# Kernel tuning notes

Measured on AMD Instinct MI355X. Metric: run time of the kernel, lower is better.

The kernel has to match this reference:

```python
import jax, jax.numpy as jnp
import numpy as np

N_HEADS = 16
HEAD_DIM = 64
ROPE_BASE = 10000.0


def _apply_rope(x, offset):
    # x: (B, T, H, hd); rotates consecutive pairs (x[2i], x[2i+1]) as complex numbers,
    # matching torch.view_as_complex on reshape(..., -1, 2).
    B, T, H, hd = x.shape
    inv_freq = 1.0 / (ROPE_BASE ** (jnp.arange(0, hd, 2, dtype=jnp.float32) / hd))  # (hd/2,)
    t = jnp.arange(T, dtype=jnp.float32) + offset
    ang = t[:, None] * inv_freq[None, :]                      # (T, hd/2)
    cos = jnp.cos(ang)[None, :, None, :]                      # (1, T, 1, hd/2)
    sin = jnp.sin(ang)[None, :, None, :]
    x1 = x[..., 0::2]
    x2 = x[..., 1::2]
    out = jnp.stack([x1 * cos - x2 * sin, x1 * sin + x2 * cos], axis=-1)
    return out.reshape(B, T, H, hd).astype(x.dtype)


def setup_inputs() -> dict:
    key = jax.random.key(0)
    ks = jax.random.split(key, 5)
    D = N_HEADS * HEAD_DIM  # 1024
    s = 1.0 / np.sqrt(D)
    x = jax.random.normal(ks[0], (2, 2048, D), jnp.float32)
    Wqkv = jax.random.normal(ks[1], (D, 3 * D), jnp.float32) * s
    bqkv = jax.random.normal(ks[2], (3 * D,), jnp.float32) * 0.01
    Wout = jax.random.normal(ks[3], (D, D), jnp.float32) * s
    bout = jax.random.normal(ks[4], (D,), jnp.float32) * 0.01
    return {"x": x, "Wqkv": Wqkv, "bqkv": bqkv, "Wout": Wout, "bout": bout, "offset": 0}


def reference(x, Wqkv, bqkv, Wout, bout, offset):
    B, T, D = x.shape
    qkv = (x @ Wqkv + bqkv).reshape(B, T, 3, N_HEADS, HEAD_DIM)
    q, k, v = qkv[:, :, 0], qkv[:, :, 1], qkv[:, :, 2]       # (B, T, H, hd)
    q = _apply_rope(q, offset)
    k = _apply_rope(k, offset)
    # kv_cache is None and T == window_size, so no crop occurs.
    new_cache = jnp.stack([k, v], axis=1)                     # (B, 2, T, H, hd)
    scale = 1.0 / np.sqrt(HEAD_DIM)
    scores = jnp.einsum("bqhd,bkhd->bhqk", q, k) * scale      # (B, H, T, T)
    mask = jnp.tril(jnp.ones((T, T), dtype=bool))
    scores = jnp.where(mask[None, None], scores, jnp.finfo(scores.dtype).min)
    attn = jax.nn.softmax(scores, axis=-1)
    ctx = jnp.einsum("bhqk,bkhd->bqhd", attn, v).reshape(B, T, D)
    out = ctx @ Wout + bout
    return (out, new_cache)
```

## Files before the change

### kernel.cpp

```cpp
#include <hip/hip_runtime.h>
#include <stdint.h>
#include <math.h>


typedef __bf16 bf16_t;
typedef bf16_t bf16x8 __attribute__((ext_vector_type(8)));
typedef float f32x4 __attribute__((ext_vector_type(4)));
typedef unsigned short ushort8_t __attribute__((ext_vector_type(8)));

__device__ __forceinline__ unsigned short f2bf(float f) {
    union { float f; unsigned int i; } v; v.f = f;
    unsigned int r = v.i + 0x7fffu + ((v.i >> 16) & 1u);
    return (unsigned short)(r >> 16);
}
__device__ __forceinline__ bf16x8 ld8(const unsigned short* p) {
    return *(const bf16x8*)p;
}
__device__ __forceinline__ void gload_lds16(const unsigned short* g, unsigned short* l) {
    __builtin_amdgcn_global_load_lds(
        (__attribute__((address_space(1))) void*)(g),
        (__attribute__((address_space(3))) void*)(l),
        16, 0, 0);
}

__global__ void k_cvt(const float* __restrict__ in, unsigned short* __restrict__ out) {
    const int i = (blockIdx.x * 256 + threadIdx.x) * 8;
    float4 a = *(const float4*)&in[i];
    float4 b = *(const float4*)&in[i + 4];
    ushort8_t v;
    v[0] = f2bf(a.x); v[1] = f2bf(a.y); v[2] = f2bf(a.z); v[3] = f2bf(a.w);
    v[4] = f2bf(b.x); v[5] = f2bf(b.y); v[6] = f2bf(b.z); v[7] = f2bf(b.w);
    *(ushort8_t*)&out[i] = v;
}

__global__ void k_ropetab(float* __restrict__ tab, const int* __restrict__ offp) {
    int idx = blockIdx.x * blockDim.x + threadIdx.x;
    int t = idx >> 5, i = idx & 31;
    float off = (float)(*offp);
    float inv = powf(10000.0f, -(float)(2 * i) / 64.0f);
    float ang = ((float)t + off) * inv;
    float s, c;
    sincosf(ang, &s, &c);
    tab[idx * 2]     = c;
    tab[idx * 2 + 1] = s;
}

__global__ void k_transposeF2B(const float* __restrict__ in,
                               unsigned short* __restrict__ out, int R, int C) {
    __shared__ __align__(16) float tile[64 * 68];
    const int bz = blockIdx.z;
    const size_t base = (size_t)bz * R * C;
    const int tR = blockIdx.y * 64, tC = blockIdx.x * 64;
    const int tid = threadIdx.x;
#pragma unroll
    for (int it = 0; it < 4; ++it) {
        int flat = (it * 256 + tid) * 4;
        int r = flat >> 6, c = flat & 63;
        *(float4*)&tile[r * 68 + c] =
            *(const float4*)&in[base + (size_t)(tR + r) * C + tC + c];
    }
    __syncthreads();
#pragma unroll
    for (int it = 0; it < 2; ++it) {
        int flat = (it * 256 + tid) * 8;
        int rr = flat >> 6, cc = flat & 63;
        ushort8_t v;
#pragma unroll
        for (int j = 0; j < 8; ++j) v[j] = f2bf(tile[(cc + j) * 68 + rr]);
        *(ushort8_t*)&out[base + (size_t)(tC + rr) * R + tR + cc] = v;
    }
}

__global__ void k_transpose64(const unsigned short* __restrict__ in,
                              unsigned short* __restrict__ out, int R, int C) {
    __shared__ __align__(16) unsigned short tile[64 * 72];
    const int bz = blockIdx.z;
    const size_t base = (size_t)bz * R * C;
    const int tR = blockIdx.y * 64, tC = blockIdx.x * 64;
    const int tid = threadIdx.x;
#pragma unroll
    for (int it = 0; it < 2; ++it) {
        int flat = (it * 256 + tid) * 8;
        int r = flat >> 6, c = flat & 63;
        *(ushort8_t*)&tile[r * 72 + c] =
            *(const ushort8_t*)&in[base + (size_t)(tR + r) * C + tC + c];
    }
    __syncthreads();
#pragma unroll
    for (int it = 0; it < 2; ++it) {
        int flat = (it * 256 + tid) * 8;
        int rr = flat >> 6, cc = flat & 63;
        ushort8_t v;
#pragma unroll
        for (int j = 0; j < 8; ++j) v[j] = tile[(cc + j) * 72 + rr];
        *(ushort8_t*)&out[base + (size_t)(tC + rr) * R + tR + cc] = v;
    }
}

template <int EPI>
__global__ __launch_bounds__(512, 2) void k_gemm(
    const unsigned short* __restrict__ A,
    const unsigned short* __restrict__ Bt,
    const float* __restrict__ bias,
    const float* __restrict__ tab,
    unsigned short* __restrict__ oq,
    unsigned short* __restrict__ ok,
    unsigned short* __restrict__ ov,
    float* __restrict__ cache,
    float* __restrict__ outp)
{
    constexpr int K = 1024;
    __shared__ __align__(16) unsigned short lds[65536];
    unsigned short* lA = lds;
    unsigned short* lB = lds + 32768;

    const int tid  = threadIdx.x;
    const int lane = tid & 63, w = tid >> 6;
    const int wr = w >> 2, wc = w & 3;
    const int lrow = lane & 15, quad = lane >> 4;

    const int gx  = gridDim.x;
    const int nwg = gx * gridDim.y;
    const int bid = blockIdx.y * gx + blockIdx.x;
    const int sw  = (bid & 7) * (nwg >> 3) + (bid >> 3);
    const int blockM = (sw / gx) * 256;
    const int blockN = (sw % gx) * 256;

    const int q8    = (lane & 7) ^ (lane >> 3);
    const int srow0 = ((w * 16 + (lane >> 3)) << 1) + ((q8 >> 2) & 1);
    const int scol  = (q8 & 3) * 8;
    const unsigned short* srcA = A  + (size_t)(blockM + srow0) * K + scol;
    const unsigned short* srcB = Bt + (size_t)(blockN + srow0) * K + scol;
    unsigned short* dA = lA + w * 1024;
    unsigned short* dB = lB + w * 1024;

    const int rp   = lrow >> 1;
    const int swzu = ((((lane & 1) << 6) | (quad << 4)) ^ (rp << 4)) >> 1;

    f32x4 acc[8][4];
#pragma unroll
    for (int m = 0; m < 8; ++m)
#pragma unroll
        for (int n = 0; n < 4; ++n) acc[m][n] = (f32x4){0.f, 0.f, 0.f, 0.f};

#define STAGE_A(T, KH) do { \
        const unsigned short* s_ = srcA + (T) * 64 + (KH) * 32; \
        unsigned short* d_ = dA + (((2*(T)+(KH)) & 3) << 13); \
        gload_lds16(s_, d_); \
        gload_lds16(s_ + 16 * K, d_ + 512); } while (0)
#define STAGE_B(T, KH) do { \
        const unsigned short* s_ = srcB + (T) * 64 + (KH) * 32; \
        unsigned short* d_ = dB + (((2*(T)+(KH)) & 3) << 13); \
        gload_lds16(s_, d_); \
        gload_lds16(s_ + 16 * K, d_ + 512); } while (0)
#define WAITN(n) asm volatile("s_waitcnt vmcnt(" #n ")" ::: "memory")
#define RD_A(slot) do { \
        _Pragma("unroll") \
        for (int m = 0; m < 8; ++m) \
            aA[m] = ld8(&lA[((slot) << 13) + (wr * 64 + m * 8 + rp) * 64 + swzu]); } while (0)
#define RD_B(slot, nh) do { \
        _Pragma("unroll") \
        for (int nl = 0; nl < 2; ++nl) \
            bB[nl] = ld8(&lB[((slot) << 13) + (wc * 32 + (nh) * 16 + nl * 8 + rp) * 64 + swzu]); } while (0)
#define MFMA16(nh) do { \
        __builtin_amdgcn_s_barrier(); \
        asm volatile("s_waitcnt lgkmcnt(0)" ::: "memory"); \
        __builtin_amdgcn_sched_barrier(0); \
        __builtin_amdgcn_s_setprio(1); \
        _Pragma("unroll") \
        for (int m = 0; m < 8; ++m) { \
            acc[m][(nh)*2+0] = __builtin_amdgcn_mfma_f32_16x16x32_bf16(aA[m], bB[0], acc[m][(nh)*2+0], 0, 0, 0); \
            acc[m][(nh)*2+1] = __builtin_amdgcn_mfma_f32_16x16x32_bf16(aA[m], bB[1], acc[m][(nh)*2+1], 0, 0, 0); } \
        __builtin_amdgcn_s_setprio(0); \
        __builtin_amdgcn_s_barrier(); } while (0)

    STAGE_A(0, 0); STAGE_B(0, 0);
    STAGE_A(0, 1); STAGE_B(0, 1);
    STAGE_A(1, 0); STAGE_B(1, 0);
    STAGE_A(1, 1);
    asm volatile("s_waitcnt vmcnt(8)" ::: "memory");
    __builtin_amdgcn_s_barrier();

    bf16x8 aA[8], bB[2];
    for (int i = 0; i < 7; ++i) {
        const int E = 2 * i, O = 2 * i + 1;
        WAITN(6); RD_A(0); RD_B(0, 0); STAGE_B(O, 1);     MFMA16(0);
        RD_B(0, 1);                    STAGE_A(E + 2, 0); MFMA16(1);
        RD_A(1); RD_B(1, 0);           STAGE_B(E + 2, 0); MFMA16(0);
        RD_B(1, 1);                    STAGE_A(E + 2, 1); MFMA16(1);
        WAITN(6); RD_A(2); RD_B(2, 0); STAGE_B(E + 2, 1); MFMA16(0);
        RD_B(2, 1);                    STAGE_A(O + 2, 0); MFMA16(1);
        RD_A(3); RD_B(3, 0);           STAGE_B(O + 2, 0); MFMA16(0);
        RD_B(3, 1);                    STAGE_A(O + 2, 1); MFMA16(1);
    }
    WAITN(6); RD_A(0); RD_B(0, 0); STAGE_B(15, 1); MFMA16(0);
    RD_B(0, 1);                                    MFMA16(1);
    RD_A(1); RD_B(1, 0);                           MFMA16(0);
    RD_B(1, 1);                                    MFMA16(1);
    WAITN(0); RD_A(2); RD_B(2, 0);                 MFMA16(0);
    RD_B(2, 1);                                    MFMA16(1);
    RD_A(3); RD_B(3, 0);                           MFMA16(0);
    RD_B(3, 1);                                    MFMA16(1);
#undef STAGE_A
#undef STAGE_B
#undef WAITN
#undef RD_A
#undef RD_B
#undef MFMA16

#pragma unroll
    for (int m = 0; m < 8; ++m) {
        const int rbase = blockM + wr * 128 + m * 16 + quad * 4;
#pragma unroll
        for (int n = 0; n < 4; ++n) {
            const int gcol = blockN + wc * 64 + n * 16 + lrow;
            const float bv = bias[gcol];
#pragma unroll
            for (int r = 0; r < 4; ++r) {
                const int row = rbase + r;
                float val = acc[m][n][r] + bv;
                if (EPI == 0) {
                    outp[(size_t)row * 1024 + gcol] = val;
                } else {
                    const int s = gcol >> 10;
                    const int cn = gcol & 1023;
                    const int h = cn >> 6, d = cn & 63;
                    const int b = row >> 11, t = row & 2047;
                    if (s < 2) {
                        const int ii = d >> 1;
                        const float cz = tab[t * 64 + 2 * ii];
                        const float sz = tab[t * 64 + 2 * ii + 1];
                        const float pv = __shfl_xor(val, 1);
                        val = (d & 1) ? (pv * sz + val * cz) : (val * cz - pv * sz);
                    }
                    const unsigned short r16 = f2bf(val);
                    const size_t bhtd = (((size_t)(b * 16 + h)) * 2048 + t) * 64 + d;
                    if (s == 0) {
                        oq[bhtd] = r16;
                    } else if (s == 1) {
                        ok[bhtd] = r16;
                        cache[(((size_t)(b * 2 + 0)) * 2048 + t) * 1024 + h * 64 + d] = val;
                    } else {
                        ov[bhtd] = r16;
                        cache[(((size_t)(b * 2 + 1)) * 2048 + t) * 1024 + h * 64 + d] = val;
                    }
                }
            }
        }
    }
}

__global__ __launch_bounds__(512, 2) void k_attn(
    const unsigned short* __restrict__ qh,
    const unsigned short* __restrict__ kh,
    const unsigned short* __restrict__ vt,
    unsigned short* __restrict__ ctx)
{
    __shared__ __align__(16) unsigned short lK[4][64 * 64];
    __shared__ __align__(16) unsigned short lV[4][64 * 64];
    __shared__ __align__(16) unsigned short lP[8][32 * 68];
    const int tid = threadIdx.x;
    const int wave = tid >> 6, lane = tid & 63;
    const int lrow = lane & 15, quad = lane >> 4;
    const int sub = lane >> 3, g8 = lane & 7;
    const int grp = g8 ^ (sub & 7);
    const int pj = blockIdx.x;
    const int h = blockIdx.y, b = blockIdx.z;
    const unsigned short* Q  = qh + (size_t)(b * 16 + h) * 2048 * 64;
    const unsigned short* Kp = kh + (size_t)(b * 16 + h) * 2048 * 64;
    const unsigned short* Vt = vt + (size_t)(b * 16 + h) * 64 * 2048;

    const int grpq = wave >> 2;
    const int wv   = wave & 3;
    const int qb   = grpq ? pj : (15 - pj);
    const int qw   = qb * 128 + wv * 32;
    const int nT   = 2 * (16 - pj);

    bf16x8 bOnes;
#pragma unroll
    for (int j = 0; j < 8; ++j) bOnes[j] = (bf16_t)1.0f;

    bf16x8 aQ[2][2];
#pragma unroll
    for (int mf = 0; mf < 2; ++mf)
#pragma unroll
        for (int ks = 0; ks < 2; ++ks) {
            bf16x8 t = ld8(&Q[(size_t)(qw + mf * 16 + lrow) * 64 + ks * 32 + quad * 8]);
#pragma unroll
            for (int j = 0; j < 8; ++j) t[j] = (bf16_t)((float)t[j] * 0.125f);
            aQ[mf][ks] = t;
        }

    f32x4 o[2][4];
#pragma unroll
    for (int mf = 0; mf < 2; ++mf)
#pragma unroll
        for (int i = 0; i < 4; ++i) o[mf][i] = (f32x4){0.f, 0.f, 0.f, 0.f};
    f32x4 lacc[2];
    lacc[0] = (f32x4){0.f, 0.f, 0.f, 0.f};
    lacc[1] = (f32x4){0.f, 0.f, 0.f, 0.f};

#define STAGE_T(t) do { \
        const int c_ = wave, s_ = (t) & 3; \
        gload_lds16(&Kp[(size_t)((t) * 64 + c_ * 8 + sub) * 64 + grp * 8], &lK[s_][c_ * 512]); \
        gload_lds16(&Vt[(size_t)(c_ * 8 + sub) * 2048 + (t) * 64 + grp * 8], &lV[s_][c_ * 512]); } while (0)

    STAGE_T(0);
    STAGE_T(1);

    for (int it = 0; it < nT; ++it) {
        if (it + 2 < nT) {
            STAGE_T(it + 2);
            asm volatile("s_waitcnt vmcnt(4)" ::: "memory");
        } else if (it + 1 < nT) {
            asm volatile("s_waitcnt vmcnt(2)" ::: "memory");
        } else {
            asm volatile("s_waitcnt vmcnt(0)" ::: "memory");
        }
        __builtin_amdgcn_s_barrier();
        __builtin_amdgcn_sched_barrier(0);
        const int kt0 = it * 64;
        if (kt0 < qw + 32) {
            const unsigned short* lKb = lK[it & 3];
            const unsigned short* lVb = lV[it & 3];
            f32x4 s[2][4];
#pragma unroll
            for (int mf = 0; mf < 2; ++mf)
#pragma unroll
                for (int i = 0; i < 4; ++i) s[mf][i] = (f32x4){0.f, 0.f, 0.f, 0.f};
            __builtin_amdgcn_s_setprio(1);
#pragma unroll
            for (int nt = 0; nt < 4; ++nt) {
                const int row = nt * 16 + lrow;
#pragma unroll
                for (int ks = 0; ks < 2; ++ks) {
                    bf16x8 bK = ld8(&lKb[row * 64 + (((ks * 4 + quad) ^ (row & 7)) * 8)]);
#pragma unroll
                    for (int mf = 0; mf < 2; ++mf)
                        s[mf][nt] = __builtin_amdgcn_mfma_f32_16x16x32_bf16(
                            aQ[mf][ks], bK, s[mf][nt], 0, 0, 0);
                }
            }
            __builtin_amdgcn_s_setprio(0);
            if (kt0 + 63 > qw) {
#pragma unroll
                for (int mf = 0; mf < 2; ++mf)
#pragma unroll
                    for (int nt = 0; nt < 4; ++nt) {
                        const int colg = kt0 + nt * 16 + lrow;
#pragma unroll
                        for (int r = 0; r < 4; ++r) {
                            const int rowg = qw + mf * 16 + quad * 4 + r;
                            const float pv = (colg <= rowg) ? __expf(s[mf][nt][r]) : 0.f;
                            lP[wave][(mf * 16 + quad * 4 + r) * 68 + nt * 16 + lrow] = f2bf(pv);
                        }
                    }
            } else {
#pragma unroll
                for (int mf = 0; mf < 2; ++mf)
#pragma unroll
                    for (int nt = 0; nt < 4; ++nt)
#pragma unroll
                        for (int r = 0; r < 4; ++r)
                            lP[wave][(mf * 16 + quad * 4 + r) * 68 + nt * 16 + lrow] =
                                f2bf(__expf(s[mf][nt][r]));
            }
            bf16x8 aP[2][2];
#pragma unroll
            for (int mf = 0; mf < 2; ++mf)
#pragma unroll
                for (int ks = 0; ks < 2; ++ks)
                    aP[mf][ks] = ld8(&lP[wave][(mf * 16 + lrow) * 68 + ks * 32 + quad * 8]);
            __builtin_amdgcn_s_setprio(1);
#pragma unroll
            for (int mf = 0; mf < 2; ++mf)
#pragma unroll
                for (int ks = 0; ks < 2; ++ks)
                    lacc[mf] = __builtin_amdgcn_mfma_f32_16x16x32_bf16(
                        aP[mf][ks], bOnes, lacc[mf], 0, 0, 0);
#pragma unroll
            for (int dt = 0; dt < 4; ++dt) {
                const int row = dt * 16 + lrow;
#pragma unroll
                for (int ks = 0; ks < 2; ++ks) {
                    bf16x8 bV = ld8(&lVb[row * 64 + (((ks * 4 + quad) ^ (row & 7)) * 8)]);
#pragma unroll
                    for (int mf = 0; mf < 2; ++mf)
                        o[mf][dt] = __builtin_amdgcn_mfma_f32_16x16x32_bf16(
                            aP[mf][ks], bV, o[mf][dt], 0, 0, 0);
                }
            }
            __builtin_amdgcn_s_setprio(0);
        }
    }
#undef STAGE_T

    float inv[2][4];
#pragma unroll
    for (int mf = 0; mf < 2; ++mf)
#pragma unroll
        for (int r = 0; r < 4; ++r) inv[mf][r] = 1.0f / lacc[mf][r];
#pragma unroll
    for (int mf = 0; mf < 2; ++mf)
#pragma unroll
        for (int dt = 0; dt < 4; ++dt) {
            const int col = h * 64 + dt * 16 + lrow;
#pragma unroll
            for (int r = 0; r < 4; ++r) {
                const int trow = qw + mf * 16 + quad * 4 + r;
                ctx[((size_t)(b * 2048 + trow)) * 1024 + col] = f2bf(o[mf][dt][r] * inv[mf][r]);
            }
        }
}

extern "C" void kernel_launch(void* const* d_in, const int* in_sizes, int n_in,
                              void* d_out, int out_size, void* d_ws, size_t ws_size,
                              hipStream_t stream) {
    (void)in_sizes; (void)n_in; (void)out_size; (void)ws_size;
    const float* x    = (const float*)d_in[0];
    const float* wqkv = (const float*)d_in[1];
    const float* bqkv = (const float*)d_in[2];
    const float* wout = (const float*)d_in[3];
    const float* bout = (const float*)d_in[4];
    const int*   offp = (const int*)d_in[5];

    float* out   = (float*)d_out;
    float* cache = out + (size_t)2 * 2048 * 1024;

    char* w = (char*)d_ws;
    float* tab            = (float*)w;          w += (size_t)2048 * 64 * sizeof(float);
    unsigned short* xb    = (unsigned short*)w; w += (size_t)4194304 * 2;
    unsigned short* wqkvT = (unsigned short*)w; w += (size_t)3072 * 1024 * 2;
    unsigned short* woutT = (unsigned short*)w; w += (size_t)1024 * 1024 * 2;
    unsigned short* qh    = (unsigned short*)w; w += (size_t)4194304 * 2;
    unsigned short* kh    = (unsigned short*)w; w += (size_t)4194304 * 2;
    unsigned short* vh    = (unsigned short*)w; w += (size_t)4194304 * 2;
    unsigned short* vt    = (unsigned short*)w; w += (size_t)4194304 * 2;
    unsigned short* ctx   = (unsigned short*)w; w += (size_t)4194304 * 2;

    k_ropetab<<<dim3(256), dim3(256), 0, stream>>>(tab, offp);
    k_cvt<<<dim3(2048), dim3(256), 0, stream>>>(x, xb);
    k_transposeF2B<<<dim3(48, 16, 1), dim3(256), 0, stream>>>(wqkv, wqkvT, 1024, 3072);
    k_transposeF2B<<<dim3(16, 16, 1), dim3(256), 0, stream>>>(wout, woutT, 1024, 1024);
    k_gemm<1><<<dim3(12, 16), dim3(512), 0, stream>>>(xb, wqkvT, bqkv, tab, qh, kh, vh, cache, nullptr);
    k_transpose64<<<dim3(1, 32, 32), dim3(256), 0, stream>>>(vh, vt, 2048, 64);
    k_attn<<<dim3(8, 16, 2), dim3(512), 0, stream>>>(qh, kh, vt, ctx);
    k_gemm<0><<<dim3(4, 16), dim3(512), 0, stream>>>(ctx, woutT, bout, tab, nullptr, nullptr, nullptr, nullptr, out);
}
```

Measured before the change: 250.2 us.

## Use inline-asm LDS reads with explicit waitcnt pipelining in GEMM and attention

Replaces compiler-generated LDS loads with inline ds_read_b128 and manual lgkmcnt waits. In the attention kernel, K and V fragments are double-buffered so the next tile's reads overlap the current MFMAs. In the GEMM, the vmcnt waits move to the end of the MFMA phase so they overlap the barrier. The inline asm hides the LDS dependencies from the compiler, so correctness now depends on every manual wait count being right, and scheduling flexibility is reduced.

Result: no change. 249.9 us (-0.1%).

```diff
diff --git a/kernel.cpp b/kernel.cpp
--- a/kernel.cpp
+++ b/kernel.cpp
@@ -15,6 +15,13 @@
 }
 __device__ __forceinline__ bf16x8 ld8(const unsigned short* p) {
     return *(const bf16x8*)p;
+}
+__device__ __forceinline__ bf16x8 lds_rd128(const unsigned short* p) {
+    bf16x8 r;
+    asm volatile("ds_read_b128 %0, %1"
+                 : "=v"(r)
+                 : "v"((const __attribute__((address_space(3))) unsigned short*)p));
+    return r;
 }
 __device__ __forceinline__ void gload_lds16(const unsigned short* g, unsigned short* l) {
     __builtin_amdgcn_global_load_lds(
@@ -22,6 +29,8 @@
         (__attribute__((address_space(3))) void*)(l),
         16, 0, 0);
 }
+#define LGK(n) asm volatile("s_waitcnt lgkmcnt(" #n ")" ::: "memory")
+#define WAITN(n) asm volatile("s_waitcnt vmcnt(" #n ")" ::: "memory")
 
 __global__ void k_cvt(const float* __restrict__ in, unsigned short* __restrict__ out) {
     const int i = (blockIdx.x * 256 + threadIdx.x) * 8;
@@ -153,16 +162,15 @@
         unsigned short* d_ = dB + (((2*(T)+(KH)) & 3) << 13); \
         gload_lds16(s_, d_); \
         gload_lds16(s_ + 16 * K, d_ + 512); } while (0)
-#define WAITN(n) asm volatile("s_waitcnt vmcnt(" #n ")" ::: "memory")
 #define RD_A(slot) do { \
         _Pragma("unroll") \
         for (int m = 0; m < 8; ++m) \
-            aA[m] = ld8(&lA[((slot) << 13) + (wr * 64 + m * 8 + rp) * 64 + swzu]); } while (0)
+            aA[m] = lds_rd128(&lA[((slot) << 13) + (wr * 64 + m * 8 + rp) * 64 + swzu]); } while (0)
 #define RD_B(slot, nh) do { \
         _Pragma("unroll") \
         for (int nl = 0; nl < 2; ++nl) \
-            bB[nl] = ld8(&lB[((slot) << 13) + (wc * 32 + (nh) * 16 + nl * 8 + rp) * 64 + swzu]); } while (0)
-#define MFMA16(nh) do { \
+            bB[nl] = lds_rd128(&lB[((slot) << 13) + (wc * 32 + (nh) * 16 + nl * 8 + rp) * 64 + swzu]); } while (0)
+#define MFMA16(nh, W) do { \
         __builtin_amdgcn_s_barrier(); \
         asm volatile("s_waitcnt lgkmcnt(0)" ::: "memory"); \
         __builtin_amdgcn_sched_barrier(0); \
@@ -172,38 +180,38 @@
             acc[m][(nh)*2+0] = __builtin_amdgcn_mfma_f32_16x16x32_bf16(aA[m], bB[0], acc[m][(nh)*2+0], 0, 0, 0); \
             acc[m][(nh)*2+1] = __builtin_amdgcn_mfma_f32_16x16x32_bf16(aA[m], bB[1], acc[m][(nh)*2+1], 0, 0, 0); } \
         __builtin_amdgcn_s_setprio(0); \
+        if (W == 1) { WAITN(6); } else if (W == 2) { WAITN(0); } \
         __builtin_amdgcn_s_barrier(); } while (0)
 
     STAGE_A(0, 0); STAGE_B(0, 0);
     STAGE_A(0, 1); STAGE_B(0, 1);
     STAGE_A(1, 0); STAGE_B(1, 0);
     STAGE_A(1, 1);
-    asm volatile("s_waitcnt vmcnt(8)" ::: "memory");
+    WAITN(6);
     __builtin_amdgcn_s_barrier();
 
     bf16x8 aA[8], bB[2];
     for (int i = 0; i < 7; ++i) {
         const int E = 2 * i, O = 2 * i + 1;
-        WAITN(6); RD_A(0); RD_B(0, 0); STAGE_B(O, 1);     MFMA16(0);
-        RD_B(0, 1);                    STAGE_A(E + 2, 0); MFMA16(1);
-        RD_A(1); RD_B(1, 0);           STAGE_B(E + 2, 0); MFMA16(0);
-        RD_B(1, 1);                    STAGE_A(E + 2, 1); MFMA16(1);
-        WAITN(6); RD_A(2); RD_B(2, 0); STAGE_B(E + 2, 1); MFMA16(0);
-        RD_B(2, 1);                    STAGE_A(O + 2, 0); MFMA16(1);
-        RD_A(3); RD_B(3, 0);           STAGE_B(O + 2, 0); MFMA16(0);
-        RD_B(3, 1);                    STAGE_A(O + 2, 1); MFMA16(1);
-    }
-    WAITN(6); RD_A(0); RD_B(0, 0); STAGE_B(15, 1); MFMA16(0);
-    RD_B(0, 1);                                    MFMA16(1);
-    RD_A(1); RD_B(1, 0);                           MFMA16(0);
-    RD_B(1, 1);                                    MFMA16(1);
-    WAITN(0); RD_A(2); RD_B(2, 0);                 MFMA16(0);
-    RD_B(2, 1);                                    MFMA16(1);
-    RD_A(3); RD_B(3, 0);                           MFMA16(0);
-    RD_B(3, 1);                                    MFMA16(1);
+        RD_A(0); RD_B(0, 0); STAGE_B(O, 1);     MFMA16(0, 0);
+        RD_B(0, 1);          STAGE_A(E + 2, 0); MFMA16(1, 0);
+        RD_A(1); RD_B(1, 0); STAGE_B(E + 2, 0); MFMA16(0, 0);
+        RD_B(1, 1);          STAGE_A(E + 2, 1); MFMA16(1, 1);
+        RD_A(2); RD_B(2, 0); STAGE_B(E + 2, 1); MFMA16(0, 0);
+        RD_B(2, 1);          STAGE_A(O + 2, 0); MFMA16(1, 0);
+        RD_A(3); RD_B(3, 0); STAGE_B(O + 2, 0); MFMA16(0, 0);
+        RD_B(3, 1);          STAGE_A(O + 2, 1); MFMA16(1, 1);
+    }
+    RD_A(0); RD_B(0, 0); STAGE_B(15, 1); MFMA16(0, 0);
+    RD_B(0, 1);                          MFMA16(1, 0);
+    RD_A(1); RD_B(1, 0);                 MFMA16(0, 0);
+    RD_B(1, 1);                          MFMA16(1, 2);
+    RD_A(2); RD_B(2, 0);                 MFMA16(0, 0);
+    RD_B(2, 1);                          MFMA16(1, 0);
+    RD_A(3); RD_B(3, 0);                 MFMA16(0, 0);
+    RD_B(3, 1);                          MFMA16(1, 0);
 #undef STAGE_A
 #undef STAGE_B
-#undef WAITN
 #undef RD_A
 #undef RD_B
 #undef MFMA16
@@ -311,11 +319,11 @@
     for (int it = 0; it < nT; ++it) {
         if (it + 2 < nT) {
             STAGE_T(it + 2);
-            asm volatile("s_waitcnt vmcnt(4)" ::: "memory");
+            WAITN(4);
         } else if (it + 1 < nT) {
-            asm volatile("s_waitcnt vmcnt(2)" ::: "memory");
+            WAITN(2);
         } else {
-            asm volatile("s_waitcnt vmcnt(0)" ::: "memory");
+            WAITN(0);
         }
         __builtin_amdgcn_s_barrier();
         __builtin_amdgcn_sched_barrier(0);
@@ -328,20 +336,30 @@
             for (int mf = 0; mf < 2; ++mf)
 #pragma unroll
                 for (int i = 0; i < 4; ++i) s[mf][i] = (f32x4){0.f, 0.f, 0.f, 0.f};
-            __builtin_amdgcn_s_setprio(1);
+            bf16x8 bK[2][2];
+            bK[0][0] = lds_rd128(&lKb[lrow * 64 + ((quad ^ (lrow & 7)) * 8)]);
+            bK[0][1] = lds_rd128(&lKb[lrow * 64 + (((4 + quad) ^ (lrow & 7)) * 8)]);
 #pragma unroll
             for (int nt = 0; nt < 4; ++nt) {
-                const int row = nt * 16 + lrow;
-#pragma unroll
-                for (int ks = 0; ks < 2; ++ks) {
-                    bf16x8 bK = ld8(&lKb[row * 64 + (((ks * 4 + quad) ^ (row & 7)) * 8)]);
+                const int cur = nt & 1;
+                if (nt < 3) {
+                    const int row = (nt + 1) * 16 + lrow;
+                    bK[cur ^ 1][0] = lds_rd128(&lKb[row * 64 + ((quad ^ (row & 7)) * 8)]);
+                    bK[cur ^ 1][1] = lds_rd128(&lKb[row * 64 + (((4 + quad) ^ (row & 7)) * 8)]);
+                    LGK(2);
+                } else {
+                    LGK(0);
+                }
+                __builtin_amdgcn_sched_barrier(0);
+                __builtin_amdgcn_s_setprio(1);
+#pragma unroll
+                for (int ks = 0; ks < 2; ++ks)
 #pragma unroll
                     for (int mf = 0; mf < 2; ++mf)
                         s[mf][nt] = __builtin_amdgcn_mfma_f32_16x16x32_bf16(
-                            aQ[mf][ks], bK, s[mf][nt], 0, 0, 0);
-                }
+                            aQ[mf][ks], bK[cur][ks], s[mf][nt], 0, 0, 0);
+                __builtin_amdgcn_s_setprio(0);
             }
-            __builtin_amdgcn_s_setprio(0);
             if (kt0 + 63 > qw) {
 #pragma unroll
                 for (int mf = 0; mf < 2; ++mf)
@@ -366,11 +384,12 @@
                                 f2bf(__expf(s[mf][nt][r]));
             }
             bf16x8 aP[2][2];
-#pragma unroll
-            for (int mf = 0; mf < 2; ++mf)
-#pragma unroll
-                for (int ks = 0; ks < 2; ++ks)
-                    aP[mf][ks] = ld8(&lP[wave][(mf * 16 + lrow) * 68 + ks * 32 + quad * 8]);
+            aP[0][0] = lds_rd128(&lP[wave][(lrow) * 68 + quad * 8]);
+            aP[0][1] = lds_rd128(&lP[wave][(lrow) * 68 + 32 + quad * 8]);
+            aP[1][0] = lds_rd128(&lP[wave][(16 + lrow) * 68 + quad * 8]);
+            aP[1][1] = lds_rd128(&lP[wave][(16 + lrow) * 68 + 32 + quad * 8]);
+            LGK(0);
+            __builtin_amdgcn_sched_barrier(0);
             __builtin_amdgcn_s_setprio(1);
 #pragma unroll
             for (int mf = 0; mf < 2; ++mf)
@@ -378,19 +397,31 @@
                 for (int ks = 0; ks < 2; ++ks)
                     lacc[mf] = __builtin_amdgcn_mfma_f32_16x16x32_bf16(
                         aP[mf][ks], bOnes, lacc[mf], 0, 0, 0);
+            __builtin_amdgcn_s_setprio(0);
+            bf16x8 bV[2][2];
+            bV[0][0] = lds_rd128(&lVb[lrow * 64 + ((quad ^ (lrow & 7)) * 8)]);
+            bV[0][1] = lds_rd128(&lVb[lrow * 64 + (((4 + quad) ^ (lrow & 7)) * 8)]);
 #pragma unroll
             for (int dt = 0; dt < 4; ++dt) {
-                const int row = dt * 16 + lrow;
-#pragma unroll
-                for (int ks = 0; ks < 2; ++ks) {
-                    bf16x8 bV = ld8(&lVb[row * 64 + (((ks * 4 + quad) ^ (row & 7)) * 8)]);
+                const int cur = dt & 1;
+                if (dt < 3) {
+                    const int row = (dt + 1) * 16 + lrow;
+                    bV[cur ^ 1][0] = lds_rd128(&lVb[row * 64 + ((quad ^ (row & 7)) * 8)]);
+                    bV[cur ^ 1][1] = lds_rd128(&lVb[row * 64 + (((4 + quad) ^ (row & 7)) * 8)]);
+                    LGK(2);
+                } else {
+                    LGK(0);
+                }
+                __builtin_amdgcn_sched_barrier(0);
+                __builtin_amdgcn_s_setprio(1);
+#pragma unroll
+                for (int ks = 0; ks < 2; ++ks)
 #pragma unroll
                     for (int mf = 0; mf < 2; ++mf)
                         o[mf][dt] = __builtin_amdgcn_mfma_f32_16x16x32_bf16(
-                            aP[mf][ks], bV, o[mf][dt], 0, 0, 0);
-                }
+                            aP[mf][ks], bV[cur][ks], o[mf][dt], 0, 0, 0);
+                __builtin_amdgcn_s_setprio(0);
             }
-            __builtin_amdgcn_s_setprio(0);
         }
     }
 #undef STAGE_T
```

## Replace output-projection GEMM with a small-tile kernel to fill more CUs

Applied to the files above, without the earlier changes.

The final projection (4096x1024 by 1024x1024) previously reused the large 256x256-tile GEMM, which launches only 64 workgroups. It now uses a new 64x64-tile kernel with 4 waves per block and a double-buffered 32-wide K loop, launching 1024 workgroups so the whole GPU is occupied. The trade-off is less data reuse per tile and a simpler pipeline without LDS swizzling, which may cost more memory traffic and LDS bank conflicts. The WAITN macro is also moved to file scope as a cleanup.

Result: faster. 243.1 us (-2.8%).

```diff
diff --git a/kernel.cpp b/kernel.cpp
--- a/kernel.cpp
+++ b/kernel.cpp
@@ -22,6 +22,7 @@
         (__attribute__((address_space(3))) void*)(l),
         16, 0, 0);
 }
+#define WAITN(n) asm volatile("s_waitcnt vmcnt(" #n ")" ::: "memory")
 
 __global__ void k_cvt(const float* __restrict__ in, unsigned short* __restrict__ out) {
     const int i = (blockIdx.x * 256 + threadIdx.x) * 8;
@@ -153,7 +154,6 @@
         unsigned short* d_ = dB + (((2*(T)+(KH)) & 3) << 13); \
         gload_lds16(s_, d_); \
         gload_lds16(s_ + 16 * K, d_ + 512); } while (0)
-#define WAITN(n) asm volatile("s_waitcnt vmcnt(" #n ")" ::: "memory")
 #define RD_A(slot) do { \
         _Pragma("unroll") \
         for (int m = 0; m < 8; ++m) \
@@ -178,7 +178,7 @@
     STAGE_A(0, 1); STAGE_B(0, 1);
     STAGE_A(1, 0); STAGE_B(1, 0);
     STAGE_A(1, 1);
-    asm volatile("s_waitcnt vmcnt(8)" ::: "memory");
+    WAITN(8);
     __builtin_amdgcn_s_barrier();
 
     bf16x8 aA[8], bB[2];
@@ -203,7 +203,6 @@
     RD_B(3, 1);                                    MFMA16(1);
 #undef STAGE_A
 #undef STAGE_B
-#undef WAITN
 #undef RD_A
 #undef RD_B
 #undef MFMA16
@@ -250,6 +249,69 @@
     }
 }
 
+__global__ __launch_bounds__(256) void k_gemm0(
+    const unsigned short* __restrict__ A,
+    const unsigned short* __restrict__ Bt,
+    const float* __restrict__ bias,
+    float* __restrict__ outp)
+{
+    constexpr int K = 1024;
+    __shared__ __align__(16) unsigned short lA[2][64 * 32];
+    __shared__ __align__(16) unsigned short lB[2][64 * 32];
+    const int tid = threadIdx.x;
+    const int wave = tid >> 6, lane = tid & 63;
+    const int lrow = lane & 15, quad = lane >> 4;
+    const int waveM = wave >> 1, waveN = wave & 1;
+    const int blockM = blockIdx.y * 64, blockN = blockIdx.x * 64;
+
+    f32x4 acc[2][2];
+#pragma unroll
+    for (int i = 0; i < 2; ++i)
+#pragma unroll
+        for (int j = 0; j < 2; ++j) acc[i][j] = (f32x4){0.f, 0.f, 0.f, 0.f};
+
+    const int srow = tid >> 2;
+    const int scol = (tid & 3) * 8;
+    auto stage = [&](int k0, int bsel) {
+        gload_lds16(&A[(size_t)(blockM + srow) * K + k0 + scol], &lA[bsel][tid * 8]);
+        gload_lds16(&Bt[(size_t)(blockN + srow) * K + k0 + scol], &lB[bsel][tid * 8]);
+    };
+
+    stage(0, 0);
+    int buf = 0;
+    for (int k0 = 0; k0 < K; k0 += 32) {
+        __syncthreads();
+        if (k0 + 32 < K) stage(k0 + 32, buf ^ 1);
+        bf16x8 af[2], bfr[2];
+#pragma unroll
+        for (int mt = 0; mt < 2; ++mt)
+            af[mt] = ld8(&lA[buf][(waveM * 32 + mt * 16 + lrow) * 32 + quad * 8]);
+#pragma unroll
+        for (int nt = 0; nt < 2; ++nt)
+            bfr[nt] = ld8(&lB[buf][(waveN * 32 + nt * 16 + lrow) * 32 + quad * 8]);
+#pragma unroll
+        for (int mt = 0; mt < 2; ++mt)
+#pragma unroll
+            for (int nt = 0; nt < 2; ++nt)
+                acc[mt][nt] = __builtin_amdgcn_mfma_f32_16x16x32_bf16(
+                    af[mt], bfr[nt], acc[mt][nt], 0, 0, 0);
+        buf ^= 1;
+    }
+
+#pragma unroll
+    for (int mt = 0; mt < 2; ++mt) {
+        const int rbase = blockM + waveM * 32 + mt * 16 + quad * 4;
+#pragma unroll
+        for (int nt = 0; nt < 2; ++nt) {
+            const int gcol = blockN + waveN * 32 + nt * 16 + lrow;
+            const float bv = bias[gcol];
+#pragma unroll
+            for (int r = 0; r < 4; ++r)
+                outp[(size_t)(rbase + r) * 1024 + gcol] = acc[mt][nt][r] + bv;
+        }
+    }
+}
+
 __global__ __launch_bounds__(512, 2) void k_attn(
     const unsigned short* __restrict__ qh,
     const unsigned short* __restrict__ kh,
@@ -311,11 +373,11 @@
     for (int it = 0; it < nT; ++it) {
         if (it + 2 < nT) {
             STAGE_T(it + 2);
-            asm volatile("s_waitcnt vmcnt(4)" ::: "memory");
+            WAITN(4);
         } else if (it + 1 < nT) {
-            asm volatile("s_waitcnt vmcnt(2)" ::: "memory");
+            WAITN(2);
         } else {
-            asm volatile("s_waitcnt vmcnt(0)" ::: "memory");
+            WAITN(0);
         }
         __builtin_amdgcn_s_barrier();
         __builtin_amdgcn_sched_barrier(0);
@@ -445,5 +507,5 @@
     k_gemm<1><<<dim3(12, 16), dim3(512), 0, stream>>>(xb, wqkvT, bqkv, tab, qh, kh, vh, cache, nullptr);
     k_transpose64<<<dim3(1, 32, 32), dim3(256), 0, stream>>>(vh, vt, 2048, 64);
     k_attn<<<dim3(8, 16, 2), dim3(512), 0, stream>>>(qh, kh, vt, ctx);
-    k_gemm<0><<<dim3(4, 16), dim3(512), 0, stream>>>(ctx, woutT, bout, tab, nullptr, nullptr, nullptr, nullptr, out);
-}
+    k_gemm0<<<dim3(16, 64), dim3(256), 0, stream>>>(ctx, woutT, bout, out);
+}
```
